# Optimization experiments

Hardware: AMD Instinct MI355X
Metric: run time of the kernel (lower is better)

Reference implementation:

```python
import jax, jax.numpy as jnp
import numpy as np
from jax import lax

# --- model constants (match init_kwargs) ---
B = 4096
T, N_FEAT = 100, 81
KH = 7                 # cnn_kernel_height
T_MOD = T - KH + 1     # 94
M = 100                # cnn_hidden_size
P = 128                # decoder hidden size
SKIP = 10
SH = 32                # skip_hidden_size
PT = T_MOD // SKIP     # 9


def setup_inputs() -> dict:
    key = jax.random.key(0)
    ks = jax.random.split(key, 18)
    s = 0.05
    def rn(k, shape, scale=s):
        return jax.random.normal(k, shape, dtype=jnp.float32) * scale
    return {
        "enc_data": jax.random.normal(ks[0], (B, T, N_FEAT), dtype=jnp.float32),
        # Conv2d(1 -> M, kernel=(KH, N_FEAT))
        "conv_w": rn(ks[1], (M, 1, KH, N_FEAT)),
        "conv_b": rn(ks[2], (M,)),
        # TemporalAttention: W_d: Linear(2P->M, no bias), U_d: Linear(M->M, no bias), v_d: Linear(M->1, no bias)
        "Wd": rn(ks[3], (M, 2 * P)),
        "Ud": rn(ks[4], (M, M)),
        "vd": rn(ks[5], (1, M)),
        # LSTM(input=M, hidden=P), PyTorch gate order i,f,g,o
        "lstm_wih": rn(ks[6], (4 * P, M)),
        "lstm_whh": rn(ks[7], (4 * P, P)),
        "lstm_bih": rn(ks[8], (4 * P,)),
        "lstm_bhh": rn(ks[9], (4 * P,)),
        # GRU(input=M, hidden=SH), PyTorch gate order r,z,n
        "gru_wih": rn(ks[10], (3 * SH, M)),
        "gru_whh": rn(ks[11], (3 * SH, SH)),
        "gru_bih": rn(ks[12], (3 * SH,)),
        "gru_bhh": rn(ks[13], (3 * SH,)),
        # output head: Linear(M+P+SKIP*SH -> P), ReLU, (Dropout=eval identity), Linear(P -> 1)
        "out1_w": rn(ks[14], (P, M + P + SKIP * SH)),
        "out1_b": rn(ks[15], (P,)),
        "out2_w": rn(ks[16], (1, P)),
        "out2_b": rn(ks[17], (1,)),
    }


def reference(enc_data, conv_w, conv_b, Wd, Ud, vd,
              lstm_wih, lstm_whh, lstm_bih, lstm_bhh,
              gru_wih, gru_whh, gru_bih, gru_bhh,
              out1_w, out1_b, out2_w, out2_b):
    b = enc_data.shape[0]

    # --- CNN encoder: Conv2d valid over full feature width -> [B, T_MOD, M] ---
    x = enc_data[:, None]  # [B,1,T,n]
    h = lax.conv_general_dilated(x, conv_w, window_strides=(1, 1), padding='VALID',
                                 dimension_numbers=('NCHW', 'OIHW', 'NCHW'))  # [B,M,T_MOD,1]
    H = jax.nn.relu(h + conv_b[None, :, None, None])[..., 0].transpose(0, 2, 1)  # [B,T_MOD,M]

    # precompute U_d(H) once (same math; U_d applied to H is step-invariant)
    HU = jnp.einsum('btm,km->btk', H, Ud)  # [B,T_MOD,M]

    def dec_step(carry, _):
        d, s = carry  # each [B,P]
        q = jnp.concatenate([d, s], axis=1)                       # [B,2P]
        e = jnp.tanh((q @ Wd.T)[:, None, :] + HU)                 # [B,T_MOD,M]
        scores = jnp.einsum('btm,m->bt', e, vd[0])                # [B,T_MOD]
        beta = jax.nn.softmax(scores, axis=1)                     # softmax over time
        c = jnp.einsum('bt,btm->bm', beta, H)                     # context [B,M]
        gates = c @ lstm_wih.T + lstm_bih + d @ lstm_whh.T + lstm_bhh
        i_g, f_g, g_g, o_g = jnp.split(gates, 4, axis=1)
        s_new = jax.nn.sigmoid(f_g) * s + jax.nn.sigmoid(i_g) * jnp.tanh(g_g)
        d_new = jax.nn.sigmoid(o_g) * jnp.tanh(s_new)
        return (d_new, s_new), (beta, c)

    d0 = jnp.zeros((b, P), dtype=enc_data.dtype)
    s0 = jnp.zeros((b, P), dtype=enc_data.dtype)
    (d_T, _), (betas, cs) = lax.scan(dec_step, (d0, s0), None, length=T_MOD)
    c_last = cs[-1]                                               # [B,M]
    dec_out = jnp.concatenate([d_T, c_last], axis=1)              # [B, P+M]

    # --- skip GRU over strided conv features ---
    Hs = H[:, -PT * SKIP:, :]                                     # [B, PT*SKIP, M]
    Hs = (Hs.transpose(0, 2, 1)                                   # [B, M, PT*SKIP]
            .reshape(b, M, PT, SKIP)
            .transpose(2, 0, 3, 1)                                # [PT, B, SKIP, M]
            .reshape(PT, b * SKIP, M))

    def gru_step(hprev, xt):
        gi = xt @ gru_wih.T + gru_bih
        gh = hprev @ gru_whh.T + gru_bhh
        ir, iz, inn = jnp.split(gi, 3, axis=1)
        hr, hz, hn = jnp.split(gh, 3, axis=1)
        r = jax.nn.sigmoid(ir + hr)
        z = jax.nn.sigmoid(iz + hz)
        nn_ = jnp.tanh(inn + r * hn)
        hnew = (1.0 - z) * nn_ + z * hprev
        return hnew, None

    h0 = jnp.zeros((b * SKIP, SH), dtype=enc_data.dtype)
    h_skip, _ = lax.scan(gru_step, h0, Hs)                        # [B*SKIP, SH]
    h_skip = h_skip.reshape(b, SKIP * SH)                         # matches torch view

    feat = jnp.concatenate([dec_out, h_skip], axis=1)             # [B, P+M+SKIP*SH]
    out = jax.nn.relu(feat @ out1_w.T + out1_b) @ out2_w.T + out2_b  # [B,1]
    return out[:, 0]
```

## Files before the change

### kernel.cpp

```cpp
#include <hip/hip_runtime.h>

typedef unsigned int u32;
typedef unsigned short u16;
typedef _Float16 half2_t __attribute__((ext_vector_type(2)));

#define TM 94
#define NB 4
#define DEC_NT 512

__device__ __forceinline__ float bf2f(u16 v){ return __builtin_bit_cast(float, ((u32)v)<<16); }
__device__ __forceinline__ float bflo(u32 v){ return __builtin_bit_cast(float, v<<16); }
__device__ __forceinline__ float bfhi(u32 v){ return __builtin_bit_cast(float, v & 0xffff0000u); }
__device__ __forceinline__ u32 f2bf_bits(float f){ u32 u=__builtin_bit_cast(u32,f); return (u + 0x7fffu + ((u>>16)&1u))>>16; }
__device__ __forceinline__ u32 packbf2(float a, float b){ return f2bf_bits(a) | (f2bf_bits(b)<<16); }
__device__ __forceinline__ u32 packh2(float a, float b){ half2_t h; h.x=(_Float16)a; h.y=(_Float16)b; return __builtin_bit_cast(u32,h); }
__device__ __forceinline__ float fdot2(u32 a, u32 b, float c){
  return __builtin_amdgcn_fdot2(__builtin_bit_cast(half2_t,a), __builtin_bit_cast(half2_t,b), c, false);
}
__device__ __forceinline__ float fast_rcp(float x){ return __builtin_amdgcn_rcpf(x); }
__device__ __forceinline__ float sigmoid_f(float x){ return fast_rcp(1.f + __expf(-x)); }
__device__ __forceinline__ float tanh_f(float x){ float e=__expf(2.f*x); return 1.f - 2.f*fast_rcp(e+1.f); }

__global__ __launch_bounds__(128)
void conv_kernel(const float* __restrict__ enc, const float* __restrict__ cw,
                 const float* __restrict__ cb, u16* __restrict__ Hb)
{
  __shared__ float sE[8100];
  const int tid = threadIdx.x;
  const int b = blockIdx.y;
  const int chunk = blockIdx.x;
  const float* ep = enc + (size_t)b*8100;
  for (int i=tid;i<8100;i+=128) sE[i]=ep[i];
  __syncthreads();
  if (tid >= TM) return;
  const int t = tid;
  const int mo = chunk*10;
  const float* wb = cw + mo*567;
  float acc[10];
  #pragma unroll
  for (int k=0;k<10;k++) acc[k]=cb[mo+k];
  const float* e = sE + t*81;
  #pragma unroll 3
  for (int j=0;j<567;j++){
    float ev = e[j];
    #pragma unroll
    for (int k=0;k<10;k++) acc[k] += ev*wb[k*567+j];
  }
  u32* out = (u32*)Hb + ((size_t)b*9400 + t*100 + mo)/2;
  #pragma unroll
  for (int k=0;k<5;k++) out[k] = packbf2(fmaxf(acc[2*k],0.f), fmaxf(acc[2*k+1],0.f));
}

#define OFF_SHU   75200
#define OFF_SQ2   152448
#define OFF_SA    154496
#define OFF_SB    156096
#define OFF_SC2   157632
#define OFF_SG    158464
#define OFF_SVD   162560
#define DEC_LDS   162960

__global__ __launch_bounds__(DEC_NT)
__attribute__((amdgpu_waves_per_eu(2, 2)))
void decoder_kernel(const u16* __restrict__ Hb, const float* __restrict__ Wd,
                    const float* __restrict__ Ud, const float* __restrict__ vd,
                    const float* __restrict__ wih, const float* __restrict__ whh,
                    const float* __restrict__ bih, const float* __restrict__ bhh,
                    float* __restrict__ dT, float* __restrict__ cLast)
{
  extern __shared__ char smem[];
  u16*      sH   = (u16*)smem;
  u16*      sHU  = (u16*)(smem + OFF_SHU);
  _Float16* sq2  = (_Float16*)(smem + OFF_SQ2);
  float*    sa   = (float*)(smem + OFF_SA);
  float*    sbeta= (float*)(smem + OFF_SB);
  u32*      sc2  = (u32*)(smem + OFF_SC2);
  _Float16* sg   = (_Float16*)(smem + OFF_SG);
  float*    svd  = (float*)(smem + OFF_SVD);

  const int tid = threadIdx.x;
  const int b0 = blockIdx.x * NB;

  {
    const uint4* src = (const uint4*)(Hb + (size_t)b0*9400);
    uint4* dst = (uint4*)sH;
    for (int i=tid;i<4700;i+=DEC_NT) dst[i]=src[i];
  }
  if (tid < 100) svd[tid] = vd[tid];
  {
    u32* q2 = (u32*)sq2;
    for (int i=tid;i<NB*128;i+=DEC_NT) q2[i]=0u;
  }
  __syncthreads();

  for (int idx=tid; idx<9400; idx+=DEC_NT){
    int kq = idx/376;
    int r  = idx - kq*376;
    int bi = r/94;
    int t  = r - 94*bi;
    const u32* hrow = (const u32*)sH + bi*4700 + t*50;
    const float* ud0 = Ud + (kq*4+0)*100;
    const float* ud1 = Ud + (kq*4+1)*100;
    const float* ud2 = Ud + (kq*4+2)*100;
    const float* ud3 = Ud + (kq*4+3)*100;
    float c0=0.f,c1=0.f,c2=0.f,c3=0.f;
    #pragma unroll 5
    for (int mq=0; mq<25; mq++){
      uint2 hp = *(const uint2*)(hrow + mq*2);
      float h0=bflo(hp.x), h1=bfhi(hp.x), h2=bflo(hp.y), h3=bfhi(hp.y);
      float4 u0 = *(const float4*)(ud0 + mq*4);
      float4 u1 = *(const float4*)(ud1 + mq*4);
      float4 u2 = *(const float4*)(ud2 + mq*4);
      float4 u3 = *(const float4*)(ud3 + mq*4);
      c0 += h0*u0.x + h1*u0.y + h2*u0.z + h3*u0.w;
      c1 += h0*u1.x + h1*u1.y + h2*u1.z + h3*u1.w;
      c2 += h0*u2.x + h1*u2.y + h2*u2.z + h3*u2.w;
      c3 += h0*u3.x + h1*u3.y + h2*u3.z + h3*u3.w;
    }
    u32* dst = (u32*)sHU + bi*4700 + t*50 + kq*2;
    dst[0] = packbf2(c0,c1);
    dst[1] = packbf2(c2,c3);
  }
  __syncthreads();

  __builtin_amdgcn_sched_barrier(0);
  const int mw = tid>>2, part = tid&3;
  u32 Wih[50]; u32 Whh[64]; u32 Wdf[32];
  float biasg;
  {
    const float2* wr = (const float2*)(wih + (size_t)tid*100);
    #pragma unroll
    for (int i=0;i<50;i++){ float2 v = wr[i]; Wih[i]=packh2(v.x,v.y); }
    const float2* hr = (const float2*)(whh + (size_t)tid*128);
    #pragma unroll
    for (int i=0;i<64;i++){ float2 v = hr[i]; Whh[i]=packh2(v.x,v.y); }
    biasg = bih[tid] + bhh[tid];
  }
  if (mw < 100){
    const float2* dr = (const float2*)(Wd + mw*256 + part*64);
    #pragma unroll
    for (int s=0;s<8;s++){
      int ii = (s+part)&7;
      #pragma unroll
      for (int k=0;k<4;k++){ float2 v = dr[ii*4+k]; Wdf[4*s+k]=packh2(v.x,v.y); }
    }
  }

  float s_reg = 0.f;

  for (int step=0; step<TM; step++){
    if (mw < 100){
      #pragma unroll
      for (int bi=0;bi<NB;bi++){
        const u32* qb = (const u32*)sq2 + bi*128 + part*32;
        float a0=0.f, a1=0.f;
        #pragma unroll
        for (int s=0;s<8;s++){
          int ii = (s+part)&7;
          uint4 qv = *(const uint4*)(qb + ii*4);
          a0 = fdot2(Wdf[4*s+0], qv.x, a0);
          a1 = fdot2(Wdf[4*s+1], qv.y, a1);
          a0 = fdot2(Wdf[4*s+2], qv.z, a0);
          a1 = fdot2(Wdf[4*s+3], qv.w, a1);
        }
        float acc = a0+a1;
        acc += __shfl_xor(acc,1);
        acc += __shfl_xor(acc,2);
        if (part==0) sa[bi*100+mw]=acc;
      }
    }
    __syncthreads();
    if (tid < 376){
      int bi = tid/94;
      int t  = tid - 94*bi;
      const u32* hu = (const u32*)sHU + bi*4700 + t*50;
      const float4* ap4 = (const float4*)(sa + bi*100);
      const float4* vp4 = (const float4*)svd;
      float acc=0.f;
      #pragma unroll
      for (int c=0;c<12;c++){
        uint4 h4 = ((const uint4*)hu)[c];
        float4 a0 = ap4[2*c], a1 = ap4[2*c+1];
        float4 v0 = vp4[2*c], v1 = vp4[2*c+1];
        acc += v0.x*tanh_f(a0.x + bflo(h4.x));
        acc += v0.y*tanh_f(a0.y + bfhi(h4.x));
        acc += v0.z*tanh_f(a0.z + bflo(h4.y));
        acc += v0.w*tanh_f(a0.w + bfhi(h4.y));
        acc += v1.x*tanh_f(a1.x + bflo(h4.z));
        acc += v1.y*tanh_f(a1.y + bfhi(h4.z));
        acc += v1.z*tanh_f(a1.z + bflo(h4.w));
        acc += v1.w*tanh_f(a1.w + bfhi(h4.w));
      }
      {
        uint2 ht = *(const uint2*)(hu + 48);
        float4 a = ap4[24]; float4 v = vp4[24];
        acc += v.x*tanh_f(a.x + bflo(ht.x));
        acc += v.y*tanh_f(a.y + bfhi(ht.x));
        acc += v.z*tanh_f(a.z + bflo(ht.y));
        acc += v.w*tanh_f(a.w + bfhi(ht.y));
      }
      sbeta[bi*96+t]=acc;
    }
    __syncthreads();
    if (tid < 64*NB){
      int bi = tid>>6, lane = tid&63;
      float s0 = sbeta[bi*96+lane];
      float s1 = (lane<30)? sbeta[bi*96+64+lane] : -1e30f;
      float mx = fmaxf(s0,s1);
      #pragma unroll
      for (int o=32;o>=1;o>>=1) mx = fmaxf(mx, __shfl_xor(mx,o));
      float e0 = __expf(s0-mx);
      float e1 = (lane<30)? __expf(s1-mx) : 0.f;
      float sm = e0+e1;
      #pragma unroll
      for (int o=32;o>=1;o>>=1) sm += __shfl_xor(sm,o);
      float rs = fast_rcp(sm);
      sbeta[bi*96+lane] = e0*rs;
      if (lane<30) sbeta[bi*96+64+lane] = e1*rs;
    }
    __syncthreads();
    if (tid < 400){
      int bi = tid/100;
      int r  = tid - 100*bi;
      int mp = r>>1, th = r&1;
      const float* bp = sbeta + bi*96 + th*47;
      const u32* hp = (const u32*)sH + bi*4700 + th*47*50 + mp;
      float a0=0.f, a1=0.f;
      #pragma unroll
      for (int i=0;i<47;i++){
        float be = bp[i];
        u32 h = hp[i*50];
        a0 += be*bflo(h); a1 += be*bfhi(h);
      }
      a0 += __shfl_xor(a0,1);
      a1 += __shfl_xor(a1,1);
      if (th==0){
        sc2[bi*52+mp] = packh2(a0,a1);
        if (step==TM-1){
          cLast[(size_t)(b0+bi)*100 + 2*mp]   = a0;
          cLast[(size_t)(b0+bi)*100 + 2*mp+1] = a1;
        }
      }
    }
    __syncthreads();
    #pragma unroll
    for (int bi=0;bi<NB;bi++){
      float a0 = biasg, a1 = 0.f;
      const uint4* cp = (const uint4*)(sc2 + bi*52);
      #pragma unroll
      for (int i=0;i<12;i++){
        uint4 cv = cp[i];
        a0 = fdot2(Wih[4*i+0], cv.x, a0);
        a1 = fdot2(Wih[4*i+1], cv.y, a1);
        a0 = fdot2(Wih[4*i+2], cv.z, a0);
        a1 = fdot2(Wih[4*i+3], cv.w, a1);
      }
      {
        const u32* ct = sc2 + bi*52 + 48;
        a0 = fdot2(Wih[48], ct[0], a0);
        a1 = fdot2(Wih[49], ct[1], a1);
      }
      const uint4* qp = (const uint4*)((const u32*)sq2 + bi*128);
      #pragma unroll
      for (int i=0;i<16;i++){
        uint4 qv = qp[i];
        a0 = fdot2(Whh[4*i+0], qv.x, a0);
        a1 = fdot2(Whh[4*i+1], qv.y, a1);
        a0 = fdot2(Whh[4*i+2], qv.z, a0);
        a1 = fdot2(Whh[4*i+3], qv.w, a1);
      }
      sg[bi*512+tid] = (_Float16)(a0+a1);
    }
    __syncthreads();
    {
      int bi = tid>>7, p = tid&127;
      float ig = (float)sg[bi*512+p];
      float fg = (float)sg[bi*512+128+p];
      float gg = (float)sg[bi*512+256+p];
      float og = (float)sg[bi*512+384+p];
      float sn = sigmoid_f(fg)*s_reg + sigmoid_f(ig)*tanh_f(gg);
      float dn = sigmoid_f(og)*tanh_f(sn);
      s_reg = sn;
      sq2[bi*256+p]=(_Float16)dn;
      sq2[bi*256+128+p]=(_Float16)sn;
      if (step==TM-1) dT[(size_t)(b0+bi)*128+p]=dn;
    }
    __syncthreads();
  }
}

__global__ __launch_bounds__(256)
void gru_kernel(const u16* __restrict__ Hb, const float* __restrict__ wih,
                const float* __restrict__ whh, const float* __restrict__ bihp,
                const float* __restrict__ bhhp, float* __restrict__ hskip)
{
  __shared__ float sWih[96][101];
  __shared__ float sWhh[96][33];
  __shared__ float sxt[8][100];
  __shared__ float sh[8][33];
  const int tid = threadIdx.x;
  for (int i=tid;i<9600;i+=256){ sWih[i/100][i%100]=wih[i]; }
  for (int i=tid;i<3072;i+=256){ sWhh[i>>5][i&31]=whh[i]; }
  const int r = tid>>5, j = tid&31;
  const int rowg = blockIdx.x*8 + r;
  const int b = rowg/10, sk = rowg - b*10;
  const float b_r = bihp[j], b_z = bihp[32+j], b_n = bihp[64+j];
  const float hb_r = bhhp[j], hb_z = bhhp[32+j], hb_n = bhhp[64+j];
  sh[r][j]=0.f;
  float h = 0.f;
  __syncthreads();
  for (int pt=0; pt<9; pt++){
    for (int i=tid;i<800;i+=256){
      int rr=i/100, m=i-rr*100;
      int rg = blockIdx.x*8+rr; int bb=rg/10, ss=rg-bb*10;
      sxt[rr][m] = bf2f(Hb[(size_t)bb*9400 + (size_t)(4+pt*10+ss)*100 + m]);
    }
    __syncthreads();
    float gi_r=b_r, gi_z=b_z, gi_n=b_n, gh_r=hb_r, gh_z=hb_z, gh_n=hb_n;
    #pragma unroll 4
    for (int m=0;m<100;m++){
      float x = sxt[r][m];
      gi_r += sWih[j][m]*x; gi_z += sWih[32+j][m]*x; gi_n += sWih[64+j][m]*x;
    }
    #pragma unroll
    for (int k=0;k<32;k++){
      float hp = sh[r][k];
      gh_r += sWhh[j][k]*hp; gh_z += sWhh[32+j][k]*hp; gh_n += sWhh[64+j][k]*hp;
    }
    float rg_ = sigmoid_f(gi_r+gh_r);
    float z  = sigmoid_f(gi_z+gh_z);
    float n  = tanh_f(gi_n + rg_*gh_n);
    h = (1.f-z)*n + z*h;
    __syncthreads();
    sh[r][j]=h;
    __syncthreads();
  }
  hskip[(size_t)b*320 + sk*32 + j] = h;
}

#define OUT_NB 32
#define OUT_LDS ((OUT_NB*552 + 8*552)*4)

__global__ __launch_bounds__(256)
void out_kernel(const float* __restrict__ dT, const float* __restrict__ cLast,
                const float* __restrict__ hskip, const float* __restrict__ w1,
                const float* __restrict__ b1, const float* __restrict__ w2,
                const float* __restrict__ b2, float* __restrict__ outp)
{
  extern __shared__ float osm[];
  float* sf = osm;
  float* sw = osm + OUT_NB*552;
  const int tid = threadIdx.x;
  const int b0 = blockIdx.x*OUT_NB;
  for (int i=tid;i<OUT_NB*548;i+=256){
    int bl = i/548, k = i - 548*bl; int b = b0+bl;
    float v;
    if (k<128) v = dT[(size_t)b*128+k];
    else if (k<228) v = cLast[(size_t)b*100+(k-128)];
    else v = hskip[(size_t)b*320+(k-228)];
    sf[bl*552+k]=v;
  }
  const int bl = tid>>3, j = tid&7;
  float outv = 0.f;
  for (int jt=0; jt<128; jt+=8){
    __syncthreads();
    for (int i=tid;i<8*548;i+=256){
      int rr=i/548, c=i-548*rr;
      sw[rr*552+c] = w1[(size_t)jt*548 + i];
    }
    __syncthreads();
    float acc = b1[jt+j];
    const float* fr = sf + bl*552;
    const float* wr = sw + j*552;
    #pragma unroll 4
    for (int k=0;k<548;k++) acc += fr[k]*wr[k];
    outv += fmaxf(acc,0.f)*w2[jt+j];
  }
  outv += __shfl_xor(outv,1);
  outv += __shfl_xor(outv,2);
  outv += __shfl_xor(outv,4);
  if (j==0) outp[b0+bl] = outv + b2[0];
}

extern "C" void kernel_launch(void* const* d_in, const int* in_sizes, int n_in,
                              void* d_out, int out_size, void* d_ws, size_t ws_size,
                              hipStream_t stream)
{
  const float* enc      = (const float*)d_in[0];
  const float* conv_w   = (const float*)d_in[1];
  const float* conv_b   = (const float*)d_in[2];
  const float* Wd       = (const float*)d_in[3];
  const float* Ud       = (const float*)d_in[4];
  const float* vd       = (const float*)d_in[5];
  const float* lstm_wih = (const float*)d_in[6];
  const float* lstm_whh = (const float*)d_in[7];
  const float* lstm_bih = (const float*)d_in[8];
  const float* lstm_bhh = (const float*)d_in[9];
  const float* gru_wih  = (const float*)d_in[10];
  const float* gru_whh  = (const float*)d_in[11];
  const float* gru_bih  = (const float*)d_in[12];
  const float* gru_bhh  = (const float*)d_in[13];
  const float* out1_w   = (const float*)d_in[14];
  const float* out1_b   = (const float*)d_in[15];
  const float* out2_w   = (const float*)d_in[16];
  const float* out2_b   = (const float*)d_in[17];

  char* ws = (char*)d_ws;
  u16*   Hb    = (u16*)ws;
  float* dT    = (float*)(ws + 77004800);
  float* cLast = (float*)(ws + 79101952);
  float* hskip = (float*)(ws + 80740352);

  conv_kernel<<<dim3(10,4096,1), 128, 0, stream>>>(enc, conv_w, conv_b, Hb);

  (void)hipFuncSetAttribute((const void*)decoder_kernel,
                            hipFuncAttributeMaxDynamicSharedMemorySize, DEC_LDS);
  decoder_kernel<<<4096/NB, DEC_NT, DEC_LDS, stream>>>(Hb, Wd, Ud, vd,
                                                       lstm_wih, lstm_whh, lstm_bih, lstm_bhh,
                                                       dT, cLast);

  gru_kernel<<<5120, 256, 0, stream>>>(Hb, gru_wih, gru_whh, gru_bih, gru_bhh, hskip);

  (void)hipFuncSetAttribute((const void*)out_kernel,
                            hipFuncAttributeMaxDynamicSharedMemorySize, OUT_LDS);
  out_kernel<<<4096/OUT_NB, 256, OUT_LDS, stream>>>(dT, cLast, hskip, out1_w, out1_b,
                                                    out2_w, out2_b, (float*)d_out);
}
```

Measured before the change: 8.340 ms.

## Restructure LSTM attention decoder with exp-factored tanh, fused gate GEMV, prepacked weights

Each decoder block now handles two samples instead of four. The hidden states are stored transposed in fp16, and the Ud projection is precomputed as exp(2x). The per-step attention tanh then becomes a multiply plus a reciprocal, with clamped exponents. Context and hidden state are packed into one vector so a single GEMV computes all LSTM gates, and the gate and Wd weights are prepacked to fp16 by a new prep kernel and streamed from global memory instead of held in registers. The conv kernel also runs two channel chunks per 256-thread block. The changes aim to cut LDS footprint (allowing more resident blocks), register pressure and transcendental work per step, at the cost of global/L2 weight traffic each step and small clamping approximations in tanh.

```diff
diff --git a/kernel.cpp b/kernel.cpp
--- a/kernel.cpp
+++ b/kernel.cpp
@@ -5,35 +5,76 @@
 typedef _Float16 half2_t __attribute__((ext_vector_type(2)));
 
 #define TM 94
-#define NB 4
+#define NB 2
 #define DEC_NT 512
 
 __device__ __forceinline__ float bf2f(u16 v){ return __builtin_bit_cast(float, ((u32)v)<<16); }
 __device__ __forceinline__ float bflo(u32 v){ return __builtin_bit_cast(float, v<<16); }
 __device__ __forceinline__ float bfhi(u32 v){ return __builtin_bit_cast(float, v & 0xffff0000u); }
-__device__ __forceinline__ u32 f2bf_bits(float f){ u32 u=__builtin_bit_cast(u32,f); return (u + 0x7fffu + ((u>>16)&1u))>>16; }
-__device__ __forceinline__ u32 packbf2(float a, float b){ return f2bf_bits(a) | (f2bf_bits(b)<<16); }
 __device__ __forceinline__ u32 packh2(float a, float b){ half2_t h; h.x=(_Float16)a; h.y=(_Float16)b; return __builtin_bit_cast(u32,h); }
 __device__ __forceinline__ float fdot2(u32 a, u32 b, float c){
   return __builtin_amdgcn_fdot2(__builtin_bit_cast(half2_t,a), __builtin_bit_cast(half2_t,b), c, false);
 }
+__device__ __forceinline__ float h2lo(u32 v){ return (float)__builtin_bit_cast(half2_t,v).x; }
+__device__ __forceinline__ float h2hi(u32 v){ return (float)__builtin_bit_cast(half2_t,v).y; }
 __device__ __forceinline__ float fast_rcp(float x){ return __builtin_amdgcn_rcpf(x); }
 __device__ __forceinline__ float sigmoid_f(float x){ return fast_rcp(1.f + __expf(-x)); }
 __device__ __forceinline__ float tanh_f(float x){ float e=__expf(2.f*x); return 1.f - 2.f*fast_rcp(e+1.f); }
 
-__global__ __launch_bounds__(128)
+__global__ __launch_bounds__(256)
+void prep_kernel(const float* __restrict__ wih, const float* __restrict__ whh,
+                 const float* __restrict__ Wd,
+                 uint4* __restrict__ Wg2, uint4* __restrict__ Wd2)
+{
+  int idx = blockIdx.x*256 + threadIdx.x;
+  if (idx < 14848){
+    int j = idx >> 9;
+    int g = idx & 511;
+    u32 r[4];
+    #pragma unroll
+    for (int s=0;s<4;s++){
+      u32 v = 0u;
+      if (j < 13){
+        int u = 4*j + s;
+        if (u < 50) v = packh2(wih[g*100+2*u], wih[g*100+2*u+1]);
+      } else {
+        int u = 4*(j-13) + s;
+        v = packh2(whh[g*128+2*u], whh[g*128+2*u+1]);
+      }
+      r[s]=v;
+    }
+    Wg2[idx] = make_uint4(r[0],r[1],r[2],r[3]);
+  } else if (idx < 18048){
+    int id2 = idx - 14848;
+    int s = id2 / 400;
+    int t = id2 - s*400;
+    int m = t >> 2, part = t & 3;
+    int ii = (s + part) & 7;
+    int base = part*32 + ii*4;
+    u32 r[4];
+    #pragma unroll
+    for (int k=0;k<4;k++){
+      int u = base + k;
+      r[k] = packh2(Wd[m*256 + 2*u], Wd[m*256 + 2*u + 1]);
+    }
+    Wd2[id2] = make_uint4(r[0],r[1],r[2],r[3]);
+  }
+}
+
+__global__ __launch_bounds__(256)
 void conv_kernel(const float* __restrict__ enc, const float* __restrict__ cw,
                  const float* __restrict__ cb, u16* __restrict__ Hb)
 {
   __shared__ float sE[8100];
   const int tid = threadIdx.x;
   const int b = blockIdx.y;
-  const int chunk = blockIdx.x;
   const float* ep = enc + (size_t)b*8100;
-  for (int i=tid;i<8100;i+=128) sE[i]=ep[i];
+  for (int i=tid;i<8100;i+=256) sE[i]=ep[i];
   __syncthreads();
-  if (tid >= TM) return;
-  const int t = tid;
+  const int sub = tid>>7;
+  const int t = tid&127;
+  if (t >= TM) return;
+  const int chunk = blockIdx.x*2 + sub;
   const int mo = chunk*10;
   const float* wb = cw + mo*567;
   float acc[10];
@@ -48,57 +89,68 @@
   }
   u32* out = (u32*)Hb + ((size_t)b*9400 + t*100 + mo)/2;
   #pragma unroll
-  for (int k=0;k<5;k++) out[k] = packbf2(fmaxf(acc[2*k],0.f), fmaxf(acc[2*k+1],0.f));
-}
-
-#define OFF_SHU   75200
-#define OFF_SQ2   152448
-#define OFF_SA    154496
-#define OFF_SB    156096
-#define OFF_SC2   157632
-#define OFF_SG    158464
-#define OFF_SVD   162560
-#define DEC_LDS   162960
+  for (int k=0;k<5;k++){
+    u32 lo = __builtin_bit_cast(u32, fmaxf(acc[2*k],0.f));
+    u32 hi = __builtin_bit_cast(u32, fmaxf(acc[2*k+1],0.f));
+    lo = (lo + 0x7fffu + ((lo>>16)&1u))>>16;
+    hi = (hi + 0x7fffu + ((hi>>16)&1u))>>16;
+    out[k] = lo | (hi<<16);
+  }
+}
+
+#define OFF_E   38400
+#define OFF_Q   76000
+#define OFF_Z   77024
+#define OFF_VD  78048
+#define OFF_U   78448
+#define DEC_LDS 80496
 
 __global__ __launch_bounds__(DEC_NT)
-__attribute__((amdgpu_waves_per_eu(2, 2)))
-void decoder_kernel(const u16* __restrict__ Hb, const float* __restrict__ Wd,
+void decoder_kernel(const u16* __restrict__ Hb, const uint4* __restrict__ Wd2,
                     const float* __restrict__ Ud, const float* __restrict__ vd,
-                    const float* __restrict__ wih, const float* __restrict__ whh,
+                    const uint4* __restrict__ Wg2,
                     const float* __restrict__ bih, const float* __restrict__ bhh,
                     float* __restrict__ dT, float* __restrict__ cLast)
 {
   extern __shared__ char smem[];
-  u16*      sH   = (u16*)smem;
-  u16*      sHU  = (u16*)(smem + OFF_SHU);
-  _Float16* sq2  = (_Float16*)(smem + OFF_SQ2);
-  float*    sa   = (float*)(smem + OFF_SA);
-  float*    sbeta= (float*)(smem + OFF_SB);
-  u32*      sc2  = (u32*)(smem + OFF_SC2);
-  _Float16* sg   = (_Float16*)(smem + OFF_SG);
-  float*    svd  = (float*)(smem + OFF_SVD);
+  _Float16* sHt  = (_Float16*)smem;
+  _Float16* sE16 = (_Float16*)(smem + OFF_E);
+  u32*      sq32 = (u32*)(smem + OFF_Q);
+  _Float16* sq16 = (_Float16*)(smem + OFF_Q);
+  u32*      sz32 = (u32*)(smem + OFF_Z);
+  _Float16* sz16 = (_Float16*)(smem + OFF_Z);
+  float*    svd  = (float*)(smem + OFF_VD);
+  float*    sa   = (float*)(smem + OFF_U);
+  float*    sbeta= (float*)(smem + OFF_U + 800);
+  u32*      sbh2 = (u32*)(smem + OFF_U + 1568);
+  _Float16* sg16 = (_Float16*)(smem + OFF_U);
 
   const int tid = threadIdx.x;
   const int b0 = blockIdx.x * NB;
 
   {
-    const uint4* src = (const uint4*)(Hb + (size_t)b0*9400);
-    uint4* dst = (uint4*)sH;
-    for (int i=tid;i<4700;i+=DEC_NT) dst[i]=src[i];
+    const u32* src = (const u32*)(Hb + (size_t)b0*9400);
+    for (int i=tid;i<9400;i+=DEC_NT){
+      int bi = i/4700; int r = i - bi*4700;
+      int t = r/50, mq = r - t*50;
+      u32 h = src[i];
+      int base = bi*9600 + (2*mq)*96 + t;
+      sHt[base]    = (_Float16)bflo(h);
+      sHt[base+96] = (_Float16)bfhi(h);
+    }
+  }
+  for (int i=tid;i<200;i+=DEC_NT){
+    int bi=i/100, m=i-bi*100;
+    *((u32*)(sHt + bi*9600 + m*96 + 94)) = 0u;
   }
   if (tid < 100) svd[tid] = vd[tid];
-  {
-    u32* q2 = (u32*)sq2;
-    for (int i=tid;i<NB*128;i+=DEC_NT) q2[i]=0u;
-  }
+  for (int i=tid;i<256;i+=DEC_NT){ sq32[i]=0u; sz32[i]=0u; }
   __syncthreads();
 
-  for (int idx=tid; idx<9400; idx+=DEC_NT){
-    int kq = idx/376;
-    int r  = idx - kq*376;
-    int bi = r/94;
-    int t  = r - 94*bi;
-    const u32* hrow = (const u32*)sH + bi*4700 + t*50;
+  for (int idx=tid; idx<4700; idx+=DEC_NT){
+    int kq = idx/188; int r = idx - kq*188;
+    int bi = r/94, t = r - bi*94;
+    const _Float16* hcol = sHt + bi*9600 + t;
     const float* ud0 = Ud + (kq*4+0)*100;
     const float* ud1 = Ud + (kq*4+1)*100;
     const float* ud2 = Ud + (kq*4+2)*100;
@@ -106,8 +158,10 @@
     float c0=0.f,c1=0.f,c2=0.f,c3=0.f;
     #pragma unroll 5
     for (int mq=0; mq<25; mq++){
-      uint2 hp = *(const uint2*)(hrow + mq*2);
-      float h0=bflo(hp.x), h1=bfhi(hp.x), h2=bflo(hp.y), h3=bfhi(hp.y);
+      float h0 = (float)hcol[(4*mq+0)*96];
+      float h1 = (float)hcol[(4*mq+1)*96];
+      float h2 = (float)hcol[(4*mq+2)*96];
+      float h3 = (float)hcol[(4*mq+3)*96];
       float4 u0 = *(const float4*)(ud0 + mq*4);
       float4 u1 = *(const float4*)(ud1 + mq*4);
       float4 u2 = *(const float4*)(ud2 + mq*4);
@@ -117,92 +171,81 @@
       c2 += h0*u2.x + h1*u2.y + h2*u2.z + h3*u2.w;
       c3 += h0*u3.x + h1*u3.y + h2*u3.z + h3*u3.w;
     }
-    u32* dst = (u32*)sHU + bi*4700 + t*50 + kq*2;
-    dst[0] = packbf2(c0,c1);
-    dst[1] = packbf2(c2,c3);
+    float e0 = __expf(2.f*fminf(fmaxf(c0,-4.f),4.f));
+    float e1 = __expf(2.f*fminf(fmaxf(c1,-4.f),4.f));
+    float e2 = __expf(2.f*fminf(fmaxf(c2,-4.f),4.f));
+    float e3 = __expf(2.f*fminf(fmaxf(c3,-4.f),4.f));
+    u32* dst = (u32*)sE16 + bi*4700 + t*50 + kq*2;
+    dst[0] = packh2(e0,e1);
+    dst[1] = packh2(e2,e3);
   }
   __syncthreads();
 
-  __builtin_amdgcn_sched_barrier(0);
   const int mw = tid>>2, part = tid&3;
-  u32 Wih[50]; u32 Whh[64]; u32 Wdf[32];
-  float biasg;
-  {
-    const float2* wr = (const float2*)(wih + (size_t)tid*100);
-    #pragma unroll
-    for (int i=0;i<50;i++){ float2 v = wr[i]; Wih[i]=packh2(v.x,v.y); }
-    const float2* hr = (const float2*)(whh + (size_t)tid*128);
-    #pragma unroll
-    for (int i=0;i<64;i++){ float2 v = hr[i]; Whh[i]=packh2(v.x,v.y); }
-    biasg = bih[tid] + bhh[tid];
-  }
-  if (mw < 100){
-    const float2* dr = (const float2*)(Wd + mw*256 + part*64);
-    #pragma unroll
-    for (int s=0;s<8;s++){
-      int ii = (s+part)&7;
-      #pragma unroll
-      for (int k=0;k<4;k++){ float2 v = dr[ii*4+k]; Wdf[4*s+k]=packh2(v.x,v.y); }
-    }
-  }
-
+  const float biasg = bih[tid] + bhh[tid];
   float s_reg = 0.f;
 
+  #pragma unroll 1
   for (int step=0; step<TM; step++){
     if (mw < 100){
+      const uint4* wp = Wd2 + tid;
+      uint4 wA = wp[0];
+      uint4 wB = wp[400];
+      float a0=0.f, a1=0.f;
       #pragma unroll
-      for (int bi=0;bi<NB;bi++){
-        const u32* qb = (const u32*)sq2 + bi*128 + part*32;
-        float a0=0.f, a1=0.f;
-        #pragma unroll
-        for (int s=0;s<8;s++){
-          int ii = (s+part)&7;
-          uint4 qv = *(const uint4*)(qb + ii*4);
-          a0 = fdot2(Wdf[4*s+0], qv.x, a0);
-          a1 = fdot2(Wdf[4*s+1], qv.y, a1);
-          a0 = fdot2(Wdf[4*s+2], qv.z, a0);
-          a1 = fdot2(Wdf[4*s+3], qv.w, a1);
-        }
-        float acc = a0+a1;
-        acc += __shfl_xor(acc,1);
-        acc += __shfl_xor(acc,2);
-        if (part==0) sa[bi*100+mw]=acc;
+      for (int s=0;s<8;s++){
+        uint4 w = wA; wA = wB;
+        if (s<6) wB = wp[(s+2)*400];
+        int ii = (s+part)&7;
+        const int qoff = part*32 + ii*4;
+        uint4 qa = *(const uint4*)(sq32 + qoff);
+        uint4 qb = *(const uint4*)(sq32 + 128 + qoff);
+        a0 = fdot2(w.x,qa.x,a0); a0 = fdot2(w.y,qa.y,a0);
+        a0 = fdot2(w.z,qa.z,a0); a0 = fdot2(w.w,qa.w,a0);
+        a1 = fdot2(w.x,qb.x,a1); a1 = fdot2(w.y,qb.y,a1);
+        a1 = fdot2(w.z,qb.z,a1); a1 = fdot2(w.w,qb.w,a1);
+      }
+      a0 += __shfl_xor(a0,1); a0 += __shfl_xor(a0,2);
+      a1 += __shfl_xor(a1,1); a1 += __shfl_xor(a1,2);
+      if (part==0){
+        sa[mw]     = __expf(2.f*fminf(fmaxf(a0,-8.f),8.f));
+        sa[100+mw] = __expf(2.f*fminf(fmaxf(a1,-8.f),8.f));
       }
     }
     __syncthreads();
     if (tid < 376){
-      int bi = tid/94;
-      int t  = tid - 94*bi;
-      const u32* hu = (const u32*)sHU + bi*4700 + t*50;
-      const float4* ap4 = (const float4*)(sa + bi*100);
-      const float4* vp4 = (const float4*)svd;
-      float acc=0.f;
+      int row = tid>>1, th = tid&1;
+      int bi = row/94, t = row - bi*94;
+      const uint2* eh = (const uint2*)((const u32*)sE16 + bi*4700 + t*50 + th*24);
+      const float4* ap = (const float4*)(sa + bi*100 + th*48);
+      const float4* vp = (const float4*)(svd + th*48);
+      float acc = 0.f;
       #pragma unroll
       for (int c=0;c<12;c++){
-        uint4 h4 = ((const uint4*)hu)[c];
-        float4 a0 = ap4[2*c], a1 = ap4[2*c+1];
-        float4 v0 = vp4[2*c], v1 = vp4[2*c+1];
-        acc += v0.x*tanh_f(a0.x + bflo(h4.x));
-        acc += v0.y*tanh_f(a0.y + bfhi(h4.x));
-        acc += v0.z*tanh_f(a0.z + bflo(h4.y));
-        acc += v0.w*tanh_f(a0.w + bfhi(h4.y));
-        acc += v1.x*tanh_f(a1.x + bflo(h4.z));
-        acc += v1.y*tanh_f(a1.y + bfhi(h4.z));
-        acc += v1.z*tanh_f(a1.z + bflo(h4.w));
-        acc += v1.w*tanh_f(a1.w + bfhi(h4.w));
-      }
-      {
-        uint2 ht = *(const uint2*)(hu + 48);
-        float4 a = ap4[24]; float4 v = vp4[24];
-        acc += v.x*tanh_f(a.x + bflo(ht.x));
-        acc += v.y*tanh_f(a.y + bfhi(ht.x));
-        acc += v.z*tanh_f(a.z + bflo(ht.y));
-        acc += v.w*tanh_f(a.w + bfhi(ht.y));
-      }
-      sbeta[bi*96+t]=acc;
-    }
-    __syncthreads();
-    if (tid < 64*NB){
+        uint2 e2 = eh[c];
+        float4 av = ap[c], vv = vp[c];
+        float r0 = fast_rcp(1.f + av.x*h2lo(e2.x));
+        float r1 = fast_rcp(1.f + av.y*h2hi(e2.x));
+        float r2 = fast_rcp(1.f + av.z*h2lo(e2.y));
+        float r3 = fast_rcp(1.f + av.w*h2hi(e2.y));
+        acc = fmaf(vv.x,r0,acc); acc = fmaf(vv.y,r1,acc);
+        acc = fmaf(vv.z,r2,acc); acc = fmaf(vv.w,r3,acc);
+      }
+      if (th){
+        uint2 e2 = eh[12];
+        float4 av = ap[12], vv = vp[12];
+        float r0 = fast_rcp(1.f + av.x*h2lo(e2.x));
+        float r1 = fast_rcp(1.f + av.y*h2hi(e2.x));
+        float r2 = fast_rcp(1.f + av.z*h2lo(e2.y));
+        float r3 = fast_rcp(1.f + av.w*h2hi(e2.y));
+        acc = fmaf(vv.x,r0,acc); acc = fmaf(vv.y,r1,acc);
+        acc = fmaf(vv.z,r2,acc); acc = fmaf(vv.w,r3,acc);
+      }
+      acc += __shfl_xor(acc,1);
+      if (!th) sbeta[bi*96+t] = -2.f*acc;
+    }
+    __syncthreads();
+    if (tid < 128){
       int bi = tid>>6, lane = tid&63;
       float s0 = sbeta[bi*96+lane];
       float s1 = (lane<30)? sbeta[bi*96+64+lane] : -1e30f;
@@ -215,74 +258,68 @@
       #pragma unroll
       for (int o=32;o>=1;o>>=1) sm += __shfl_xor(sm,o);
       float rs = fast_rcp(sm);
-      sbeta[bi*96+lane] = e0*rs;
-      if (lane<30) sbeta[bi*96+64+lane] = e1*rs;
-    }
-    __syncthreads();
-    if (tid < 400){
-      int bi = tid/100;
-      int r  = tid - 100*bi;
-      int mp = r>>1, th = r&1;
-      const float* bp = sbeta + bi*96 + th*47;
-      const u32* hp = (const u32*)sH + bi*4700 + th*47*50 + mp;
-      float a0=0.f, a1=0.f;
-      #pragma unroll
-      for (int i=0;i<47;i++){
-        float be = bp[i];
-        u32 h = hp[i*50];
-        a0 += be*bflo(h); a1 += be*bfhi(h);
-      }
-      a0 += __shfl_xor(a0,1);
-      a1 += __shfl_xor(a1,1);
-      if (th==0){
-        sc2[bi*52+mp] = packh2(a0,a1);
-        if (step==TM-1){
-          cLast[(size_t)(b0+bi)*100 + 2*mp]   = a0;
-          cLast[(size_t)(b0+bi)*100 + 2*mp+1] = a1;
+      float b0v = e0*rs;
+      float b1v = (lane<30)? e1*rs : 0.f;
+      float b0p = __shfl_xor(b0v,1);
+      float b1p = __shfl_xor(b1v,1);
+      if ((lane&1)==0){
+        sbh2[bi*48 + (lane>>1)] = packh2(b0v, b0p);
+        if (lane < 32) sbh2[bi*48 + 32 + (lane>>1)] = packh2(b1v, b1p);
+      }
+    }
+    __syncthreads();
+    if (tid < 256){
+      int bi = tid>>7, m = tid&127;
+      if (m < 100){
+        const uint4* hp = (const uint4*)(sHt + bi*9600 + m*96);
+        const uint4* bp = (const uint4*)(sbh2 + bi*48);
+        float acc=0.f;
+        #pragma unroll
+        for (int c=0;c<12;c++){
+          uint4 h4 = hp[c];
+          uint4 b4 = bp[c];
+          acc = fdot2(h4.x,b4.x,acc); acc = fdot2(h4.y,b4.y,acc);
+          acc = fdot2(h4.z,b4.z,acc); acc = fdot2(h4.w,b4.w,acc);
         }
-      }
-    }
-    __syncthreads();
-    #pragma unroll
-    for (int bi=0;bi<NB;bi++){
-      float a0 = biasg, a1 = 0.f;
-      const uint4* cp = (const uint4*)(sc2 + bi*52);
-      #pragma unroll
-      for (int i=0;i<12;i++){
-        uint4 cv = cp[i];
-        a0 = fdot2(Wih[4*i+0], cv.x, a0);
-        a1 = fdot2(Wih[4*i+1], cv.y, a1);
-        a0 = fdot2(Wih[4*i+2], cv.z, a0);
-        a1 = fdot2(Wih[4*i+3], cv.w, a1);
-      }
-      {
-        const u32* ct = sc2 + bi*52 + 48;
-        a0 = fdot2(Wih[48], ct[0], a0);
-        a1 = fdot2(Wih[49], ct[1], a1);
-      }
-      const uint4* qp = (const uint4*)((const u32*)sq2 + bi*128);
-      #pragma unroll
-      for (int i=0;i<16;i++){
-        uint4 qv = qp[i];
-        a0 = fdot2(Whh[4*i+0], qv.x, a0);
-        a1 = fdot2(Whh[4*i+1], qv.y, a1);
-        a0 = fdot2(Whh[4*i+2], qv.z, a0);
-        a1 = fdot2(Whh[4*i+3], qv.w, a1);
-      }
-      sg[bi*512+tid] = (_Float16)(a0+a1);
+        sz16[bi*256+m] = (_Float16)acc;
+        if (step==TM-1) cLast[(size_t)(b0+bi)*100+m] = acc;
+      }
     }
     __syncthreads();
     {
+      const int g = tid;
+      float accA = biasg, accB = biasg;
+      const uint4* wp5 = Wg2 + g;
+      uint4 W0 = wp5[0], W1 = wp5[512], W2 = wp5[1024], W3 = wp5[1536];
+      #pragma unroll 1
+      for (int j=0;j<29;j++){
+        uint4 w = W0; W0=W1; W1=W2; W2=W3;
+        int jn = j+4; if (jn>28) jn=28;
+        W3 = wp5[jn*512];
+        int zoff = 4*j + ((j>=13)?12:0);
+        uint4 za = *(const uint4*)(sz32 + zoff);
+        uint4 zb = *(const uint4*)(sz32 + 128 + zoff);
+        accA = fdot2(w.x,za.x,accA); accA = fdot2(w.y,za.y,accA);
+        accA = fdot2(w.z,za.z,accA); accA = fdot2(w.w,za.w,accA);
+        accB = fdot2(w.x,zb.x,accB); accB = fdot2(w.y,zb.y,accB);
+        accB = fdot2(w.z,zb.z,accB); accB = fdot2(w.w,zb.w,accB);
+      }
+      sg16[g]     = (_Float16)accA;
+      sg16[512+g] = (_Float16)accB;
+    }
+    __syncthreads();
+    if (tid < 256){
       int bi = tid>>7, p = tid&127;
-      float ig = (float)sg[bi*512+p];
-      float fg = (float)sg[bi*512+128+p];
-      float gg = (float)sg[bi*512+256+p];
-      float og = (float)sg[bi*512+384+p];
+      float ig = (float)sg16[bi*512+p];
+      float fg = (float)sg16[bi*512+128+p];
+      float gg = (float)sg16[bi*512+256+p];
+      float og = (float)sg16[bi*512+384+p];
       float sn = sigmoid_f(fg)*s_reg + sigmoid_f(ig)*tanh_f(gg);
       float dn = sigmoid_f(og)*tanh_f(sn);
       s_reg = sn;
-      sq2[bi*256+p]=(_Float16)dn;
-      sq2[bi*256+128+p]=(_Float16)sn;
+      sq16[bi*256+p]     = (_Float16)dn;
+      sq16[bi*256+128+p] = (_Float16)sn;
+      sz16[bi*256+128+p] = (_Float16)dn;
       if (step==TM-1) dT[(size_t)(b0+bi)*128+p]=dn;
     }
     __syncthreads();
@@ -410,13 +447,17 @@
   float* dT    = (float*)(ws + 77004800);
   float* cLast = (float*)(ws + 79101952);
   float* hskip = (float*)(ws + 80740352);
-
-  conv_kernel<<<dim3(10,4096,1), 128, 0, stream>>>(enc, conv_w, conv_b, Hb);
+  uint4* Wg2   = (uint4*)(ws + 80740352);
+  uint4* Wd2   = (uint4*)(ws + 80740352 + 237568);
+
+  prep_kernel<<<71, 256, 0, stream>>>(lstm_wih, lstm_whh, Wd, Wg2, Wd2);
+
+  conv_kernel<<<dim3(5,4096,1), 256, 0, stream>>>(enc, conv_w, conv_b, Hb);
 
   (void)hipFuncSetAttribute((const void*)decoder_kernel,
                             hipFuncAttributeMaxDynamicSharedMemorySize, DEC_LDS);
-  decoder_kernel<<<4096/NB, DEC_NT, DEC_LDS, stream>>>(Hb, Wd, Ud, vd,
-                                                       lstm_wih, lstm_whh, lstm_bih, lstm_bhh,
+  decoder_kernel<<<4096/NB, DEC_NT, DEC_LDS, stream>>>(Hb, Wd2, Ud, vd, Wg2,
+                                                       lstm_bih, lstm_bhh,
                                                        dT, cLast);
 
   gru_kernel<<<5120, 256, 0, stream>>>(Hb, gru_wih, gru_whh, gru_bih, gru_bhh, hskip);
```

Measured after the change: 8.780 ms. 5.3% more time.
